# Kernel tuning notes

Hardware: AMD Instinct MI355X
Metric: run time of the kernel (lower is better)

Reference implementation:

```python
import jax, jax.numpy as jnp
from jax import lax
import numpy as np

B, H, W = 1, 128, 256
C = 32           # feature_channels
D = 32           # max_disp
HID = 64         # hidden_channels in message passing
ITERS = 5


def conv2d(x, w, b):
    # x: [N, Cin, H, W], w: [Cout, Cin, kh, kw], SAME padding, stride 1
    y = lax.conv_general_dilated(x, w, (1, 1), [(1, 1), (1, 1)],
                                 dimension_numbers=('NCHW', 'OIHW', 'NCHW'))
    return y + b[None, :, None, None]


def setup_inputs() -> dict:
    key = jax.random.key(0)
    ks = jax.random.split(key, 12)
    def p(k, shape, s=0.05):
        return jax.random.normal(k, shape, jnp.float32) * s
    return {
        'left_img':  jax.random.normal(ks[0], (B, 3, H, W), jnp.float32),
        'right_img': jax.random.normal(ks[1], (B, 3, H, W), jnp.float32),
        # feature extractor (3 -> C -> C)
        'fe_w1': p(ks[2], (C, 3, 3, 3)),  'fe_b1': jnp.zeros((C,), jnp.float32),
        'fe_w2': p(ks[3], (C, C, 3, 3)),  'fe_b2': jnp.zeros((C,), jnp.float32),
        # cost volume 1x1 conv over concat(left, shifted_right): 2C -> 1
        'cv_w': p(ks[4], (2 * C,)),       'cv_b': jnp.zeros((), jnp.float32),
        # message passing: concat(feature, belief)=C+1 -> HID -> 1
        'mp_w1': p(ks[5], (HID, C + 1, 3, 3)), 'mp_b1': jnp.zeros((HID,), jnp.float32),
        'mp_w2': p(ks[6], (1, HID, 3, 3)),     'mp_b2': jnp.zeros((1,), jnp.float32),
        # refinement: concat(left_img, disparity)=4 -> 32 -> 32 -> 1 residual
        'rf_w1': p(ks[7], (32, 4, 3, 3)),  'rf_b1': jnp.zeros((32,), jnp.float32),
        'rf_w2': p(ks[8], (32, 32, 3, 3)), 'rf_b2': jnp.zeros((32,), jnp.float32),
        'rf_w3': p(ks[9], (1, 32, 3, 3)),  'rf_b3': jnp.zeros((1,), jnp.float32),
    }


def _forward(left_img, right_img, fe_w1, fe_b1, fe_w2, fe_b2, cv_w, cv_b,
             mp_w1, mp_b1, mp_w2, mp_b2, rf_w1, rf_b1, rf_w2, rf_b2, rf_w3, rf_b3):
    def feat(img):
        h = jax.nn.relu(conv2d(img, fe_w1, fe_b1))
        return jax.nn.relu(conv2d(h, fe_w2, fe_b2))

    lf = feat(left_img)    # [B, C, H, W]
    rf = feat(right_img)   # [B, C, H, W]

    # Cost volume: shift right features by each disparity, 1x1 conv on concat.
    rf_sh = jnp.stack([jnp.pad(rf, ((0, 0), (0, 0), (0, 0), (d, 0)))[..., :W]
                       for d in range(D)])                     # [D, B, C, H, W]
    pair = jnp.concatenate([jnp.broadcast_to(lf[None], rf_sh.shape), rf_sh], axis=2)  # [D,B,2C,H,W]
    cost = jnp.einsum('dbchw,c->dbhw', pair, cv_w) + cv_b      # [D, B, H, W]
    data = cost[:, :, None]                                     # [D, B, 1, H, W]

    # Iterative BP message passing, vectorized across all disparity planes.
    def mp(data_term):  # data_term: [B, 1, H, W]
        def step(belief, _):
            x = jnp.concatenate([lf, belief], axis=1)           # [B, C+1, H, W]
            hdn = jax.nn.relu(conv2d(x, mp_w1, mp_b1))          # [B, HID, H, W]
            msg = conv2d(hdn, mp_w2, mp_b2)                     # [B, 1, H, W]
            return data_term + msg, None
        belief, _ = lax.scan(step, data_term, None, length=ITERS)
        return belief

    beliefs = jax.vmap(mp)(data)                                # [D, B, 1, H, W]
    refined = jnp.transpose(beliefs, (1, 2, 0, 3, 4))           # [B, 1, D, H, W]

    prob = jax.nn.softmax(-refined, axis=2)                     # [B, 1, D, H, W]
    idx = jnp.arange(D, dtype=prob.dtype)
    disparity = jnp.einsum('bodhw,d->bohw', prob, idx)          # [B, 1, H, W]

    # Refinement network (residual).
    x = jnp.concatenate([left_img, disparity], axis=1)          # [B, 4, H, W]
    r = jax.nn.relu(conv2d(x, rf_w1, rf_b1))
    r = jax.nn.relu(conv2d(r, rf_w2, rf_b2))
    res = conv2d(r, rf_w3, rf_b3)
    return disparity + res                                      # [B, 1, H, W]


def reference(left_img, right_img, fe_w1, fe_b1, fe_w2, fe_b2, cv_w, cv_b,
              mp_w1, mp_b1, mp_w2, mp_b2, rf_w1, rf_b1, rf_w2, rf_b2, rf_w3, rf_b3):
    return _forward(left_img, right_img, fe_w1, fe_b1, fe_w2, fe_b2, cv_w, cv_b,
                    mp_w1, mp_b1, mp_w2, mp_b2, rf_w1, rf_b1, rf_w2, rf_b2, rf_w3, rf_b3)
```

## Files before the change

### kernel.cpp

```cpp
#include <hip/hip_runtime.h>
#include <hip/hip_bf16.h>

#define H 128
#define W 256
#define HW (H*W)
#define NC 32
#define ND 32
#define NHID 64

__global__ __launch_bounds__(256) void conv3x3(
        const float* __restrict__ in0, const float* __restrict__ in1,
        float* __restrict__ out0, float* __restrict__ out1,
        const float* __restrict__ w, const float* __restrict__ b,
        int CIN, int COUT, int wstride, int dorelu,
        const float* __restrict__ addin) {
    __shared__ float wS[2304];
    __shared__ float tile[2][4][10][35];
    const int tid = threadIdx.x;
    const int zg = (COUT + 7) >> 3;
    const int img = blockIdx.z / zg;
    const int cog = blockIdx.z % zg;
    const float* in = img ? in1 : in0;
    float* out = img ? out1 : out0;
    const int cobase = cog * 8;
    int nco = COUT - cobase; if (nco > 8) nco = 8;
    const int gx0 = blockIdx.x * 32, gy0 = blockIdx.y * 8;
    const int tx = tid & 31, ty = tid >> 5;

    const int wcnt = nco * CIN * 9;
    for (int i = tid; i < wcnt; i += 256) {
        int co = i / (CIN * 9), rem = i % (CIN * 9);
        wS[i] = w[(size_t)(cobase + co) * wstride + rem];
    }

    const int nst = (CIN + 3) >> 2;
    {
        int nch = CIN < 4 ? CIN : 4;
        for (int i = tid; i < nch * 340; i += 256) {
            int ch = i / 340, rem = i % 340;
            int r = rem / 34, cc = rem % 34;
            int gy = gy0 + r - 1, gx = gx0 + cc - 1;
            tile[0][ch][r][cc] = (gy >= 0 && gy < H && gx >= 0 && gx < W)
                                 ? in[(size_t)ch * HW + gy * W + gx] : 0.f;
        }
    }
    __syncthreads();

    float acc[8];
#pragma unroll
    for (int i = 0; i < 8; i++) acc[i] = 0.f;

    for (int s = 0; s < nst; s++) {
        const int c0 = s * 4;
        int nch = CIN - c0; if (nch > 4) nch = 4;
        if (s + 1 < nst) {
            const int c1 = c0 + 4;
            int nch2 = CIN - c1; if (nch2 > 4) nch2 = 4;
            const int nb = (s + 1) & 1;
            for (int i = tid; i < nch2 * 340; i += 256) {
                int ch = i / 340, rem = i % 340;
                int r = rem / 34, cc = rem % 34;
                int gy = gy0 + r - 1, gx = gx0 + cc - 1;
                tile[nb][ch][r][cc] = (gy >= 0 && gy < H && gx >= 0 && gx < W)
                                      ? in[(size_t)(c1 + ch) * HW + gy * W + gx] : 0.f;
            }
        }
        const int cb = s & 1;
        for (int ch = 0; ch < nch; ch++) {
            float v[9];
#pragma unroll
            for (int ky = 0; ky < 3; ky++)
#pragma unroll
                for (int kx = 0; kx < 3; kx++)
                    v[ky * 3 + kx] = tile[cb][ch][ty + ky][tx + kx];
            const int wb = (c0 + ch) * 9;
#pragma unroll
            for (int co = 0; co < 8; co++) {
                if (co < nco) {
                    const float* wp = &wS[co * CIN * 9 + wb];
#pragma unroll
                    for (int k = 0; k < 9; k++) acc[co] += wp[k] * v[k];
                }
            }
        }
        __syncthreads();
    }

    const int gy = gy0 + ty, gx = gx0 + tx;
    const float ad = addin ? addin[gy * W + gx] : 0.f;
#pragma unroll
    for (int co = 0; co < 8; co++) {
        if (co < nco) {
            float r = acc[co] + b[cobase + co];
            if (dorelu) r = fmaxf(r, 0.f);
            r += ad;
            out[(size_t)(cobase + co) * HW + gy * W + gx] = r;
        }
    }
}

__global__ void chan_dot(const float* __restrict__ lf, const float* __restrict__ rf,
                         const float* __restrict__ cvw,
                         float* __restrict__ lsum, float* __restrict__ rsum) {
    int p = blockIdx.x * 256 + threadIdx.x;
    if (p >= HW) return;
    float ls = 0.f, rs = 0.f;
    for (int c = 0; c < NC; c++) {
        ls += lf[c * HW + p] * cvw[c];
        rs += rf[c * HW + p] * cvw[NC + c];
    }
    lsum[p] = ls;
    rsum[p] = rs;
}

__global__ void cost_expand(const float* __restrict__ lsum, const float* __restrict__ rsum,
                            const float* __restrict__ cvb,
                            float* __restrict__ cost, float* __restrict__ bel) {
    int idx = blockIdx.x * 256 + threadIdx.x;
    if (idx >= ND * HW) return;
    int d = idx / HW, p = idx % HW;
    int col = p & (W - 1);
    float c = lsum[p] + cvb[0];
    if (col >= d) c += rsum[p - d];
    cost[idx] = c;
    bel[idx] = c;
}

__global__ void a_transpose(const float* __restrict__ A, float* __restrict__ At) {
    __shared__ float t[64][65];
    int p0 = blockIdx.x * 64;
    int tx = threadIdx.x & 63;
    int ty = threadIdx.x >> 6;
#pragma unroll
    for (int r = 0; r < 16; r++) {
        int hid = ty * 16 + r;
        t[tx][hid] = A[(size_t)hid * HW + p0 + tx];
    }
    __syncthreads();
#pragma unroll
    for (int r = 0; r < 16; r++) {
        int p = ty * 16 + r;
        At[(size_t)(p0 + p) * 64 + tx] = t[p][tx];
    }
}

#define LOADROW(YC, AR)                                                        \
  {                                                                            \
    if ((YC) >= 0 && (YC) < H) {                                               \
      AR[0] = bp[e0off];                                                       \
      _Pragma("unroll") for (int j = 1; j < 17; j++) AR[j] = bp[(j - 8) * 64]; \
      AR[17] = bp[e17off];                                                     \
    }                                                                          \
    bp += W * 64;                                                              \
  }

#define LOADBEL(Z, BR)                                                         \
  {                                                                            \
    const int z_ = (Z);                                                        \
    if (z_ >= 0 && z_ < H) {                                                   \
      const float* br_ = beld + (size_t)z_ * W + x0;                           \
      BR[0] = xnot0 ? br_[-2] : 0.f;                                           \
      BR[1] = xnot0 ? br_[-1] : 0.f;                                           \
      _Pragma("unroll") for (int q = 0; q < 16; q++) BR[q + 2] = br_[q];       \
      BR[18] = xnotE ? br_[16] : 0.f;                                          \
      BR[19] = xnotE ? br_[17] : 0.f;                                          \
    } else {                                                                   \
      _Pragma("unroll") for (int q = 0; q < 20; q++) BR[q] = 0.f;              \
    }                                                                          \
  }

#define COMPUTE(U, AR, HARR, B0, B1, B2)                                       \
  {                                                                            \
    const int yc_ = y0 + (U);                                                  \
    if (yc_ < 0 || yc_ >= H) {                                                 \
      _Pragma("unroll") for (int j = 0; j < 18; j++) HARR[j] = 0.f;            \
    } else {                                                                   \
      _Pragma("unroll") for (int j = 0; j < 18; j++) {                         \
        float acc_ = AR[j];                                                    \
        acc_ += w1[0] * B0[j] + w1[1] * B0[j + 1] + w1[2] * B0[j + 2];         \
        acc_ += w1[3] * B1[j] + w1[4] * B1[j + 1] + w1[5] * B1[j + 2];         \
        acc_ += w1[6] * B2[j] + w1[7] * B2[j + 1] + w1[8] * B2[j + 2];         \
        HARR[j] = fmaxf(acc_, 0.f);                                            \
      }                                                                        \
      if (x0 == 0) HARR[0] = 0.f;                                              \
      if (x0 == W - 16) HARR[17] = 0.f;                                        \
    }                                                                          \
  }

#define EMIT3(T, HH2, HH1, HH0)                                                \
  {                                                                            \
    _Pragma("unroll") for (int jo = 0; jo < 16; jo++) {                        \
      float pp = w2[0] * HH2[jo] + w2[1] * HH2[jo + 1] + w2[2] * HH2[jo + 2]   \
               + w2[3] * HH1[jo] + w2[4] * HH1[jo + 1] + w2[5] * HH1[jo + 2]   \
               + w2[6] * HH0[jo] + w2[7] * HH0[jo + 1] + w2[8] * HH0[jo + 2];  \
      partW[jo][lane] = pp;                                                    \
    }                                                                          \
    {                                                                          \
      const float4* pr = (const float4*)&partW[pq][qq * 16];                   \
      float4 v0 = pr[0], v1 = pr[1], v2 = pr[2], v3 = pr[3];                   \
      float s_ = (((v0.x + v0.y) + (v0.z + v0.w)) +                            \
                  ((v1.x + v1.y) + (v1.z + v1.w))) +                           \
                 (((v2.x + v2.y) + (v2.z + v2.w)) +                            \
                  ((v3.x + v3.y) + (v3.z + v3.w)));                            \
      s_ += __shfl_xor(s_, 16);                                                \
      s_ += __shfl_xor(s_, 32);                                                \
      if (qq == 0) bout[obase + (size_t)(T) * W] = cst[(T)] + s_ + b2;         \
    }                                                                          \
  }

#define STEP(T, AIN, AOUT, HX2, HX1, HX0, B0, B1, B2, BN, DOLOAD, DOBEL)       \
  {                                                                            \
    if (DOBEL) { LOADBEL(y0 + (T) + 3, BN); }                                  \
    if (DOLOAD) { LOADROW(y0 + (T) + 2, AOUT); }                               \
    COMPUTE((T) + 1, AIN, HX0, B0, B1, B2);                                    \
    EMIT3(T, HX2, HX1, HX0);                                                   \
  }

__global__ __launch_bounds__(256, 1) void mp_iter_fast(
    const float* __restrict__ At,
    const float* __restrict__ cost,
    const float* __restrict__ bin,
    float* __restrict__ bout,
    const float* __restrict__ mp_w1,
    const float* __restrict__ mp_w2,
    const float* __restrict__ mp_b2) {
    __shared__ float partS[4][16][68];

    const int tid = threadIdx.x;
    const int lane = tid & 63;
    const int lw = __builtin_amdgcn_readfirstlane(tid >> 6);
    float (*partW)[68] = partS[lw];

    const int i = blockIdx.x;
    const int xcd = i & 7;
    const int jj = i >> 3;
    const int ybl = jj & 1;
    const int sl = (jj >> 1) & 15;
    const int d4 = jj >> 5;
    const int d = d4 * 4 + lw;
    const int x0 = sl * 16;
    const int y0 = (xcd + 8 * ybl) * 8;
    const bool xnot0 = (x0 > 0), xnotE = (x0 < W - 16);

    float w1[9], w2[9];
#pragma unroll
    for (int k = 0; k < 9; k++) {
        w1[k] = mp_w1[lane * 297 + 288 + k];
        w2[k] = mp_w2[lane * 9 + k];
    }
    const float b2 = mp_b2[0];

    const float* bp = At + (size_t)(y0 - 1) * (W * 64) + (x0 + 7) * 64 + lane;
    const int e0off  = (x0 == 0)      ? -448 : -512;
    const int e17off = (x0 == W - 16) ?  512 :  576;

    const float* beld = bin + (size_t)d * HW;
    const int pq = lane & 15, qq = lane >> 4;
    const size_t obase = (size_t)d * HW + (size_t)y0 * W + x0 + pq;

    float cst[8];
#pragma unroll
    for (int t = 0; t < 8; t++) cst[t] = cost[obase + (size_t)t * W];

    float aA[18], aB[18];
    float hA[18], hB[18], hC[18];
    float bl0[20], bl1[20], bl2[20], bl3[20];

    LOADBEL(y0 - 2, bl0);
    LOADBEL(y0 - 1, bl1);
    LOADBEL(y0,     bl2);
    LOADROW(y0 - 1, aA);
    LOADROW(y0,     aB);
    COMPUTE(-1, aA, hA, bl0, bl1, bl2);
    LOADBEL(y0 + 1, bl3);
    LOADROW(y0 + 1, aA);
    COMPUTE(0, aB, hB, bl1, bl2, bl3);
    LOADBEL(y0 + 2, bl0);

    STEP(0, aA, aB, hA, hB, hC, bl2, bl3, bl0, bl1, 1, 1)
    STEP(1, aB, aA, hB, hC, hA, bl3, bl0, bl1, bl2, 1, 1)
    STEP(2, aA, aB, hC, hA, hB, bl0, bl1, bl2, bl3, 1, 1)
    STEP(3, aB, aA, hA, hB, hC, bl1, bl2, bl3, bl0, 1, 1)
    STEP(4, aA, aB, hB, hC, hA, bl2, bl3, bl0, bl1, 1, 1)
    STEP(5, aB, aA, hC, hA, hB, bl3, bl0, bl1, bl2, 1, 1)
    STEP(6, aA, aB, hA, hB, hC, bl0, bl1, bl2, bl3, 1, 1)
    STEP(7, aB, aA, hB, hC, hA, bl1, bl2, bl3, bl0, 0, 0)
}

__global__ void softmax_disp(const float* __restrict__ bel, const float* __restrict__ left,
                             float* __restrict__ disp, float* __restrict__ x4) {
    int p = blockIdx.x * 256 + threadIdx.x;
    if (p >= HW) return;
    float v[ND];
    float m = -1e30f;
#pragma unroll
    for (int d = 0; d < ND; d++) {
        v[d] = -bel[d * HW + p];
        m = fmaxf(m, v[d]);
    }
    float s = 0.f, ws = 0.f;
#pragma unroll
    for (int d = 0; d < ND; d++) {
        float e = __expf(v[d] - m);
        s += e;
        ws += e * (float)d;
    }
    float dv = ws / s;
    disp[p] = dv;
    x4[3 * HW + p] = dv;
    x4[p] = left[p];
    x4[HW + p] = left[HW + p];
    x4[2 * HW + p] = left[2 * HW + p];
}

extern "C" void kernel_launch(void* const* d_in, const int* in_sizes, int n_in,
                              void* d_out, int out_size, void* d_ws, size_t ws_size,
                              hipStream_t stream) {
    const float* left   = (const float*)d_in[0];
    const float* right  = (const float*)d_in[1];
    const float* fe_w1  = (const float*)d_in[2];
    const float* fe_b1  = (const float*)d_in[3];
    const float* fe_w2  = (const float*)d_in[4];
    const float* fe_b2  = (const float*)d_in[5];
    const float* cv_w   = (const float*)d_in[6];
    const float* cv_b   = (const float*)d_in[7];
    const float* mp_w1  = (const float*)d_in[8];
    const float* mp_b1  = (const float*)d_in[9];
    const float* mp_w2  = (const float*)d_in[10];
    const float* mp_b2  = (const float*)d_in[11];
    const float* rf_w1  = (const float*)d_in[12];
    const float* rf_b1  = (const float*)d_in[13];
    const float* rf_w2  = (const float*)d_in[14];
    const float* rf_b2  = (const float*)d_in[15];
    const float* rf_w3  = (const float*)d_in[16];
    const float* rf_b3  = (const float*)d_in[17];
    float* out = (float*)d_out;

    float* ws = (float*)d_ws;
    float* At    = ws;
    float* tmp0  = ws;
    float* tmp1  = ws + 1048576;
    float* lf    = ws + 2097152;
    float* rfeat = ws + 3145728;
    float* cost  = ws + 4194304;
    float* Araw  = ws + 4194304;
    float* bel   = ws + 5242880;
    float* bel2  = ws + 6291456;
    float* lsum  = ws + 7340032;
    float* rsum  = ws + 7372800;
    float* disp  = ws + 7405568;
    float* x4    = ws + 7438336;

    dim3 blk(256);

    conv3x3<<<dim3(8, 16, 8), blk, 0, stream>>>(left, right, tmp0, tmp1, fe_w1, fe_b1, 3, 32, 27, 1, nullptr);
    conv3x3<<<dim3(8, 16, 8), blk, 0, stream>>>(tmp0, tmp1, lf, rfeat, fe_w2, fe_b2, 32, 32, 288, 1, nullptr);

    chan_dot<<<dim3(HW / 256), blk, 0, stream>>>(lf, rfeat, cv_w, lsum, rsum);

    conv3x3<<<dim3(8, 16, 8), blk, 0, stream>>>(lf, lf, Araw, Araw, mp_w1, mp_b1, 32, 64, 297, 0, nullptr);
    a_transpose<<<dim3(HW / 64), blk, 0, stream>>>(Araw, At);

    cost_expand<<<dim3(ND * HW / 256), blk, 0, stream>>>(lsum, rsum, cv_b, cost, bel);

    dim3 gmp(2048);
    mp_iter_fast<<<gmp, blk, 0, stream>>>(At, cost, bel,  bel2, mp_w1, mp_w2, mp_b2);
    mp_iter_fast<<<gmp, blk, 0, stream>>>(At, cost, bel2, bel,  mp_w1, mp_w2, mp_b2);
    mp_iter_fast<<<gmp, blk, 0, stream>>>(At, cost, bel,  bel2, mp_w1, mp_w2, mp_b2);
    mp_iter_fast<<<gmp, blk, 0, stream>>>(At, cost, bel2, bel,  mp_w1, mp_w2, mp_b2);
    mp_iter_fast<<<gmp, blk, 0, stream>>>(At, cost, bel,  bel2, mp_w1, mp_w2, mp_b2);

    softmax_disp<<<dim3(HW / 256), blk, 0, stream>>>(bel2, left, disp, x4);

    conv3x3<<<dim3(8, 16, 4), blk, 0, stream>>>(x4, x4, At, At, rf_w1, rf_b1, 4, 32, 36, 1, nullptr);
    conv3x3<<<dim3(8, 16, 4), blk, 0, stream>>>(At, At, rfeat, rfeat, rf_w2, rf_b2, 32, 32, 288, 1, nullptr);
    conv3x3<<<dim3(8, 16, 1), blk, 0, stream>>>(rfeat, rfeat, out, out, rf_w3, rf_b3, 32, 1, 288, 0, disp);
}
```

Before: 525.9 us.

## Fuse transpose into conv epilogue and merge cost kernels; raise mp occupancy

The hidden-layer conv now writes its output directly in pixel-major [HW][64] layout, which removes the separate transpose kernel and its intermediate buffer. The channel-dot and cost-expand kernels are merged into one row-per-block kernel that keeps the right sums in shared memory. In the message-passing kernel, cost values are loaded per output row instead of preloaded into registers, and launch bounds now request 8 blocks per CU instead of 1. That bound may force register spilling, since the kernel keeps large register arrays.

```diff
diff --git a/kernel.cpp b/kernel.cpp
--- a/kernel.cpp
+++ b/kernel.cpp
@@ -13,7 +13,7 @@
         float* __restrict__ out0, float* __restrict__ out1,
         const float* __restrict__ w, const float* __restrict__ b,
         int CIN, int COUT, int wstride, int dorelu,
-        const float* __restrict__ addin) {
+        const float* __restrict__ addin, int tpose) {
     __shared__ float wS[2304];
     __shared__ float tile[2][4][10][35];
     const int tid = threadIdx.x;
@@ -88,59 +88,46 @@
 
     const int gy = gy0 + ty, gx = gx0 + tx;
     const float ad = addin ? addin[gy * W + gx] : 0.f;
-#pragma unroll
-    for (int co = 0; co < 8; co++) {
-        if (co < nco) {
+    if (tpose) {
+        float* op = out + (size_t)(gy * W + gx) * 64 + cobase;
+#pragma unroll
+        for (int co = 0; co < 8; co++) {
             float r = acc[co] + b[cobase + co];
             if (dorelu) r = fmaxf(r, 0.f);
-            r += ad;
-            out[(size_t)(cobase + co) * HW + gy * W + gx] = r;
-        }
-    }
-}
-
-__global__ void chan_dot(const float* __restrict__ lf, const float* __restrict__ rf,
-                         const float* __restrict__ cvw,
-                         float* __restrict__ lsum, float* __restrict__ rsum) {
-    int p = blockIdx.x * 256 + threadIdx.x;
-    if (p >= HW) return;
+            op[co] = r + ad;
+        }
+    } else {
+#pragma unroll
+        for (int co = 0; co < 8; co++) {
+            if (co < nco) {
+                float r = acc[co] + b[cobase + co];
+                if (dorelu) r = fmaxf(r, 0.f);
+                r += ad;
+                out[(size_t)(cobase + co) * HW + gy * W + gx] = r;
+            }
+        }
+    }
+}
+
+__global__ void chan_cost(const float* __restrict__ lf, const float* __restrict__ rf,
+                          const float* __restrict__ cvw, const float* __restrict__ cvb,
+                          float* __restrict__ cost, float* __restrict__ bel) {
+    __shared__ float rsS[W];
+    const int x = threadIdx.x;
+    const int p = blockIdx.x * W + x;
     float ls = 0.f, rs = 0.f;
     for (int c = 0; c < NC; c++) {
         ls += lf[c * HW + p] * cvw[c];
         rs += rf[c * HW + p] * cvw[NC + c];
     }
-    lsum[p] = ls;
-    rsum[p] = rs;
-}
-
-__global__ void cost_expand(const float* __restrict__ lsum, const float* __restrict__ rsum,
-                            const float* __restrict__ cvb,
-                            float* __restrict__ cost, float* __restrict__ bel) {
-    int idx = blockIdx.x * 256 + threadIdx.x;
-    if (idx >= ND * HW) return;
-    int d = idx / HW, p = idx % HW;
-    int col = p & (W - 1);
-    float c = lsum[p] + cvb[0];
-    if (col >= d) c += rsum[p - d];
-    cost[idx] = c;
-    bel[idx] = c;
-}
-
-__global__ void a_transpose(const float* __restrict__ A, float* __restrict__ At) {
-    __shared__ float t[64][65];
-    int p0 = blockIdx.x * 64;
-    int tx = threadIdx.x & 63;
-    int ty = threadIdx.x >> 6;
-#pragma unroll
-    for (int r = 0; r < 16; r++) {
-        int hid = ty * 16 + r;
-        t[tx][hid] = A[(size_t)hid * HW + p0 + tx];
-    }
+    rsS[x] = rs;
+    ls += cvb[0];
     __syncthreads();
 #pragma unroll
-    for (int r = 0; r < 16; r++) {
-        int p = ty * 16 + r;
-        At[(size_t)(p0 + p) * 64 + tx] = t[p][tx];
+    for (int d = 0; d < ND; d++) {
+        float cc = ls + (x >= d ? rsS[x - d] : 0.f);
+        cost[(size_t)d * HW + p] = cc;
+        bel[(size_t)d * HW + p] = cc;
     }
 }
 
@@ -197,14 +184,16 @@
     }                                                                          \
     {                                                                          \
       const float4* pr = (const float4*)&partW[pq][qq * 16];                   \
-      float4 v0 = pr[0], v1 = pr[1], v2 = pr[2], v3 = pr[3];                   \
-      float s_ = (((v0.x + v0.y) + (v0.z + v0.w)) +                            \
-                  ((v1.x + v1.y) + (v1.z + v1.w))) +                           \
-                 (((v2.x + v2.y) + (v2.z + v2.w)) +                            \
-                  ((v3.x + v3.y) + (v3.z + v3.w)));                            \
+      float cg_ = cost[obase + (size_t)(T) * W];                               \
+      float4 v0 = pr[0], v1 = pr[1];                                           \
+      float s_ = ((v0.x + v0.y) + (v0.z + v0.w)) +                             \
+                 ((v1.x + v1.y) + (v1.z + v1.w));                              \
+      float4 v2 = pr[2], v3 = pr[3];                                           \
+      s_ += ((v2.x + v2.y) + (v2.z + v2.w)) +                                  \
+            ((v3.x + v3.y) + (v3.z + v3.w));                                   \
       s_ += __shfl_xor(s_, 16);                                                \
       s_ += __shfl_xor(s_, 32);                                                \
-      if (qq == 0) bout[obase + (size_t)(T) * W] = cst[(T)] + s_ + b2;         \
+      if (qq == 0) bout[obase + (size_t)(T) * W] = cg_ + s_ + b2;              \
     }                                                                          \
   }
 
@@ -216,7 +205,7 @@
     EMIT3(T, HX2, HX1, HX0);                                                   \
   }
 
-__global__ __launch_bounds__(256, 1) void mp_iter_fast(
+__global__ __launch_bounds__(256, 8) void mp_iter_fast(
     const float* __restrict__ At,
     const float* __restrict__ cost,
     const float* __restrict__ bin,
@@ -257,10 +246,6 @@
     const float* beld = bin + (size_t)d * HW;
     const int pq = lane & 15, qq = lane >> 4;
     const size_t obase = (size_t)d * HW + (size_t)y0 * W + x0 + pq;
-
-    float cst[8];
-#pragma unroll
-    for (int t = 0; t < 8; t++) cst[t] = cost[obase + (size_t)t * W];
 
     float aA[18], aB[18];
     float hA[18], hB[18], hC[18];
@@ -343,25 +328,19 @@
     float* lf    = ws + 2097152;
     float* rfeat = ws + 3145728;
     float* cost  = ws + 4194304;
-    float* Araw  = ws + 4194304;
     float* bel   = ws + 5242880;
     float* bel2  = ws + 6291456;
-    float* lsum  = ws + 7340032;
-    float* rsum  = ws + 7372800;
     float* disp  = ws + 7405568;
     float* x4    = ws + 7438336;
 
     dim3 blk(256);
 
-    conv3x3<<<dim3(8, 16, 8), blk, 0, stream>>>(left, right, tmp0, tmp1, fe_w1, fe_b1, 3, 32, 27, 1, nullptr);
-    conv3x3<<<dim3(8, 16, 8), blk, 0, stream>>>(tmp0, tmp1, lf, rfeat, fe_w2, fe_b2, 32, 32, 288, 1, nullptr);
-
-    chan_dot<<<dim3(HW / 256), blk, 0, stream>>>(lf, rfeat, cv_w, lsum, rsum);
-
-    conv3x3<<<dim3(8, 16, 8), blk, 0, stream>>>(lf, lf, Araw, Araw, mp_w1, mp_b1, 32, 64, 297, 0, nullptr);
-    a_transpose<<<dim3(HW / 64), blk, 0, stream>>>(Araw, At);
-
-    cost_expand<<<dim3(ND * HW / 256), blk, 0, stream>>>(lsum, rsum, cv_b, cost, bel);
+    conv3x3<<<dim3(8, 16, 8), blk, 0, stream>>>(left, right, tmp0, tmp1, fe_w1, fe_b1, 3, 32, 27, 1, nullptr, 0);
+    conv3x3<<<dim3(8, 16, 8), blk, 0, stream>>>(tmp0, tmp1, lf, rfeat, fe_w2, fe_b2, 32, 32, 288, 1, nullptr, 0);
+
+    conv3x3<<<dim3(8, 16, 8), blk, 0, stream>>>(lf, lf, At, At, mp_w1, mp_b1, 32, 64, 297, 0, nullptr, 1);
+
+    chan_cost<<<dim3(H), blk, 0, stream>>>(lf, rfeat, cv_w, cv_b, cost, bel);
 
     dim3 gmp(2048);
     mp_iter_fast<<<gmp, blk, 0, stream>>>(At, cost, bel,  bel2, mp_w1, mp_w2, mp_b2);
@@ -372,7 +351,7 @@
 
     softmax_disp<<<dim3(HW / 256), blk, 0, stream>>>(bel2, left, disp, x4);
 
-    conv3x3<<<dim3(8, 16, 4), blk, 0, stream>>>(x4, x4, At, At, rf_w1, rf_b1, 4, 32, 36, 1, nullptr);
-    conv3x3<<<dim3(8, 16, 4), blk, 0, stream>>>(At, At, rfeat, rfeat, rf_w2, rf_b2, 32, 32, 288, 1, nullptr);
-    conv3x3<<<dim3(8, 16, 1), blk, 0, stream>>>(rfeat, rfeat, out, out, rf_w3, rf_b3, 32, 1, 288, 0, disp);
-}
+    conv3x3<<<dim3(8, 16, 4), blk, 0, stream>>>(x4, x4, At, At, rf_w1, rf_b1, 4, 32, 36, 1, nullptr, 0);
+    conv3x3<<<dim3(8, 16, 4), blk, 0, stream>>>(At, At, rfeat, rfeat, rf_w2, rf_b2, 32, 32, 288, 1, nullptr, 0);
+    conv3x3<<<dim3(8, 16, 1), blk, 0, stream>>>(rfeat, rfeat, out, out, rf_w3, rf_b3, 32, 1, 288, 0, disp, 0);
+}
```

Result: slower. 954.8 us (+81.5%).
